# Kernel optimization log

Measured on AMD Instinct MI355X. Metric: run time of the kernel, lower is better.

Reference implementation:

```python
import jax, jax.numpy as jnp
import numpy as np

N = 1048576   # nodes (1024x1024 fluid grid)
E = 8388608   # edges (avg degree 8)
IDX_NODE_X, IDX_NODE_Y = 0, 1
IDX_EDGE_X, IDX_EDGE_Y = 0, 1


def setup_inputs() -> dict:
    key = jax.random.key(0)
    ks = jax.random.split(key, 9)
    v_x = jax.random.normal(ks[0], (N, 2), jnp.float32)
    v_prev_x = jax.random.normal(ks[1], (N, 2), jnp.float32)
    p_x = jax.random.normal(ks[2], (N, 1), jnp.float32)
    p_prev_x = jax.random.normal(ks[3], (N, 1), jnp.float32)
    rho_x = jax.random.normal(ks[4], (N, 1), jnp.float32)
    rho_prev_x = jax.random.normal(ks[5], (N, 1), jnp.float32)
    edge_attr = jax.random.normal(ks[6], (E, 2), jnp.float32)
    # mimic grid finite-difference sparsity: ~half the entries of each
    # direction column are exactly zero, exercising the != 0 edge masking
    keep = jax.random.bernoulli(ks[7], 0.5, (E, 2))
    edge_attr = jnp.where(keep, edge_attr, 0.0)
    edge_index = jax.random.randint(ks[8], (2, E), 0, N, dtype=jnp.int64)
    return dict(
        v_x=v_x, v_prev_x=v_prev_x, p_x=p_x, p_prev_x=p_prev_x,
        rho_x=rho_x, rho_prev_x=rho_prev_x,
        M=jnp.float32(1.0), eta=jnp.float32(1.0), zeta=jnp.float32(1.0),
        dt=jnp.float32(0.01), edge_attr=edge_attr, edge_index=edge_index,
    )


def _spatial_derivative(x, src, dst, edge_attr, mask, idx_node, idx_edge, n):
    """Gather-compute-scatter finite difference: scatter-mean of
    (x[dst, idx_node] - x[src, idx_node]) / edge_attr[:, idx_edge]
    over the masked edge subset, aggregated at the source node."""
    diff = x[dst, idx_node] - x[src, idx_node]                  # [E]
    denom = jnp.where(mask, edge_attr[:, idx_edge], 1.0)        # avoid /0 on masked-out edges
    contrib = jnp.where(mask, diff / denom, 0.0)                # [E]
    sums = jax.ops.segment_sum(contrib, src, num_segments=n)    # [N]
    cnt = jax.ops.segment_sum(mask.astype(x.dtype), src, num_segments=n)
    return sums / jnp.maximum(cnt, 1.0)                         # [N]


def reference(v_x, v_prev_x, p_x, p_prev_x, rho_x, rho_prev_x, M, eta, zeta, dt, edge_attr, edge_index):
    n = v_x.shape[0]
    src, dst = edge_index[0], edge_index[1]
    vp = v_x * p_x                                  # [N,2] * [N,1] -> [N,2]
    mask_x = edge_attr[:, IDX_NODE_X] != 0          # edges with x-offset
    mask_y = edge_attr[:, IDX_NODE_Y] != 0          # edges with y-offset
    d_x = _spatial_derivative(vp, src, dst, edge_attr, mask_x, IDX_NODE_X, IDX_EDGE_X, n)
    d_y = _spatial_derivative(vp, src, dst, edge_attr, mask_y, IDX_NODE_Y, IDX_EDGE_Y, n)
    loss_continuity = (d_x + d_y)[:, None] + (p_x - p_prev_x) / dt   # [N,1]
    return loss_continuity
```

## Files before the change

### kernel.cpp

```cpp
#include <hip/hip_runtime.h>
#include <hip/hip_fp16.h>


#define NPB      2048
#define NPB_LOG  11
#define NBUCK_MAX 512
#define CE       4096
#define CB       1024
#define EPT      4
#define CCAP     4608
#define MAXCHUNK 2048
#define NHINT    4096
#define SPILLCAP (1 << 20)
#define K_OFF    1073741824.0

typedef unsigned long long ull;
typedef float vfloat2 __attribute__((ext_vector_type(2)));


__global__ void node_pre_fast(const float2* __restrict__ v,
                              const float* __restrict__ p,
                              __half2* __restrict__ vph,
                              int* __restrict__ spill_cnt, int N) {
    int i = blockIdx.x * blockDim.x + threadIdx.x;
    int stride = gridDim.x * blockDim.x;
    for (; i < N; i += stride) {
        float2 vi = v[i];
        float pi = p[i];
        vph[i] = __float22half2_rn(make_float2(vi.x * pi, vi.y * pi));
    }
    if (blockIdx.x == 0 && threadIdx.x == 0) *spill_cnt = 0;
}

__device__ __forceinline__ void route_rec(uint2 r, int k, size_t rb, int slot,
                                          uint2* __restrict__ recs,
                                          uint4* __restrict__ spill,
                                          int* __restrict__ spill_cnt) {
    if (slot < CCAP) { recs[rb + slot] = r; return; }
    int sp = atomicAdd(spill_cnt, 1);
    if (sp < SPILLCAP) spill[sp] = make_uint4(r.x, r.y, (unsigned)k, 0u);
}

__global__ __launch_bounds__(CB) void chunk_sort(
        const float2* __restrict__ ea,
        const int* __restrict__ src_idx,
        const int* __restrict__ dst_idx,
        uint2* __restrict__ recs,
        unsigned short* __restrict__ off_mat,
        unsigned short* __restrict__ cnt_mat,
        uint4* __restrict__ spill,
        int* __restrict__ spill_cnt,
        int nbuck, int E) {
    __shared__ uint2 stage[CCAP];
    __shared__ int hist[NBUCK_MAX];
    __shared__ int tl[NBUCK_MAX];
    __shared__ int cur[NBUCK_MAX];
    int c = blockIdx.x, t = threadIdx.x;
    int e0 = c * CE;

    uint2 R0[EPT], R1[EPT];
    int K[EPT], NR[EPT];
#pragma unroll
    for (int i = 0; i < EPT; ++i) {
        int e = e0 + i * CB + t;
        NR[i] = 0; K[i] = 0;
        if (e < E) {
            float2 a = ea[e];
            bool mx = (a.x != 0.f);
            bool my = (a.y != 0.f);
            if (mx || my) {
                int s = src_idx[e];
                int d = dst_idx[e];
                K[i] = s >> NPB_LOG;
                unsigned sl = (unsigned)(s & (NPB - 1));
                unsigned dm = (unsigned)d << 12;
                NR[i] = (int)mx + (int)my;
                uint2 rx = make_uint2(sl | dm, __float_as_uint(a.x));
                uint2 ry = make_uint2(sl | 0x800u | dm, __float_as_uint(a.y));
                R0[i] = mx ? rx : ry;
                R1[i] = ry;
            }
        }
    }
    if (t < nbuck) hist[t] = 0;
    __syncthreads();
#pragma unroll
    for (int i = 0; i < EPT; ++i)
        if (NR[i]) atomicAdd(&hist[K[i]], NR[i]);
    __syncthreads();
    if (t < nbuck) tl[t] = hist[t];
    __syncthreads();
    for (int off = 1; off < NBUCK_MAX; off <<= 1) {
        int x = 0;
        if (t < nbuck && t >= off) x = tl[t - off];
        __syncthreads();
        if (t < nbuck) tl[t] += x;
        __syncthreads();
    }
    int total = tl[nbuck - 1];
    if (t < nbuck) {
        int excl = tl[t] - hist[t];
        cur[t] = excl;
        off_mat[(size_t)c * nbuck + t] = (unsigned short)excl;
        cnt_mat[(size_t)c * nbuck + t] = (unsigned short)hist[t];
    }
    __syncthreads();
    size_t rb = (size_t)c * CCAP;
    if (total <= CCAP) {
#pragma unroll
        for (int i = 0; i < EPT; ++i)
            if (NR[i]) {
                int slot = atomicAdd(&cur[K[i]], NR[i]);
                stage[slot] = R0[i];
                if (NR[i] == 2) stage[slot + 1] = R1[i];
            }
        __syncthreads();
        for (int j = t; j < total; j += CB) recs[rb + j] = stage[j];
    } else {
#pragma unroll
        for (int i = 0; i < EPT; ++i)
            if (NR[i]) {
                int slot = atomicAdd(&cur[K[i]], NR[i]);
                route_rec(R0[i], K[i], rb, slot, recs, spill, spill_cnt);
                if (NR[i] == 2) route_rec(R1[i], K[i], rb, slot + 1, recs, spill, spill_cnt);
            }
    }
}

__global__ __launch_bounds__(1024) void bucket_reduce(
        const uint2* __restrict__ recs,
        const unsigned short* __restrict__ off_mat,
        const unsigned short* __restrict__ cnt_mat,
        const float2* __restrict__ v,
        const float* __restrict__ p,
        const __half2* __restrict__ vph,
        const uint4* __restrict__ spill,
        const int* __restrict__ spill_cnt,
        const float* __restrict__ p_prev,
        const float* __restrict__ dt_ptr,
        float* __restrict__ out,
        int nchunk, int nbuck, int N) {
    __shared__ float2 vps[NPB];
    __shared__ double2 acc[NPB];
    __shared__ int glen[MAXCHUNK];
    __shared__ int goff[MAXCHUNK];
    __shared__ unsigned short hint[NHINT];
    __shared__ int s_sp;
    int k = blockIdx.x, t = threadIdx.x;
    int g0 = k * NPB;
    const vfloat2* vv = (const vfloat2*)v;
    for (int i = t; i < NPB; i += 1024) {
        int g = g0 + i;
        vfloat2 vi = (g < N) ? __builtin_nontemporal_load(&vv[g]) : (vfloat2)(0.f);
        float pi = (g < N) ? __builtin_nontemporal_load(&p[g]) : 0.f;
        vps[i] = make_float2(vi.x * pi, vi.y * pi);
        acc[i] = make_double2(0.0, 0.0);
    }
    if (t == 0) s_sp = *spill_cnt;
    for (int c = t; c < MAXCHUNK; c += 1024) {
        int len = 0, off = 0;
        if (c < nchunk) {
            off = __builtin_nontemporal_load(&off_mat[(size_t)c * nbuck + k]);
            int cnt = __builtin_nontemporal_load(&cnt_mat[(size_t)c * nbuck + k]);
            len = min(cnt, max(0, CCAP - off));
        }
        goff[c] = off;
        glen[c] = len;
    }
    __syncthreads();
    for (int off = 1; off < MAXCHUNK; off <<= 1) {
        int i0 = t, i1 = t + 1024;
        int x0 = (i0 >= off) ? glen[i0 - off] : 0;
        int x1 = glen[i1 - off];
        __syncthreads();
        glen[i0] += x0;
        glen[i1] += x1;
        __syncthreads();
    }
    int total = glen[MAXCHUNK - 1];
    int nh = min((total + 7) >> 3, NHINT);
    for (int j = t; j < nh; j += 1024) {
        int target = j << 3;
        int lo = 0, hi = nchunk - 1;
        while (lo < hi) {
            int mid = (lo + hi) >> 1;
            if (glen[mid] > target) hi = mid; else lo = mid + 1;
        }
        hint[j] = (unsigned short)lo;
    }
    __syncthreads();
    const ull* recs64 = (const ull*)recs;
    for (int idx = t; idx < total; idx += 1024) {
        int cur = hint[idx >> 3];
        while (glen[cur] <= idx) ++cur;
        int pre = cur ? glen[cur - 1] : 0;
        ull rv = __builtin_nontemporal_load(
            &recs64[(size_t)cur * CCAP + goff[cur] + (idx - pre)]);
        unsigned m = (unsigned)rv;
        float a = __uint_as_float((unsigned)(rv >> 32));
        int sl = (int)(m & (NPB - 1u));
        bool diry = (m >> 11) & 1u;
        int d = (int)(m >> 12);
        float2 vpd = __half22float2(vph[d]);
        float2 vs = vps[sl];
        float c = (diry ? vpd.y - vs.y : vpd.x - vs.x) / a;
        unsafeAtomicAdd(diry ? &acc[sl].y : &acc[sl].x, (double)c + K_OFF);
    }
    __syncthreads();
    int nsp = min(s_sp, SPILLCAP);
    for (int i = t; i < nsp; i += 1024) {
        uint4 r = spill[i];
        if ((int)r.z != k) continue;
        unsigned m = r.x;
        float a = __uint_as_float(r.y);
        int sl = (int)(m & (NPB - 1u));
        bool diry = (m >> 11) & 1u;
        int d = (int)(m >> 12);
        float2 vpd = __half22float2(vph[d]);
        float2 vs = vps[sl];
        float c = (diry ? vpd.y - vs.y : vpd.x - vs.x) / a;
        unsafeAtomicAdd(diry ? &acc[sl].y : &acc[sl].x, (double)c + K_OFF);
    }
    if (nsp) __syncthreads();
    float inv_dt = 1.0f / dt_ptr[0];
    for (int i = t; i < NPB; i += 1024) {
        int g = g0 + i;
        if (g < N) {
            double2 A = acc[i];
            double cx = rint(A.x * (1.0 / K_OFF));
            double sx = A.x - cx * K_OFF;
            double cy = rint(A.y * (1.0 / K_OFF));
            double sy = A.y - cy * K_OFF;
            float pd = __builtin_nontemporal_load(&p[g]);
            float pp = __builtin_nontemporal_load(&p_prev[g]);
            out[g] = (float)(sx / fmax(cx, 1.0)) + (float)(sy / fmax(cy, 1.0))
                   + (pd - pp) * inv_dt;
        }
    }
}


__global__ void fb_node_pre(const float2* __restrict__ v,
                            const float* __restrict__ p,
                            float2* __restrict__ vp,
                            double2* __restrict__ acc, int N) {
    int i = blockIdx.x * blockDim.x + threadIdx.x;
    int stride = gridDim.x * blockDim.x;
    for (; i < N; i += stride) {
        float2 vi = v[i];
        float pi = p[i];
        vp[i] = make_float2(vi.x * pi, vi.y * pi);
        acc[i] = make_double2(0.0, 0.0);
    }
}

__global__ void fb_edge_scatter(const float2* __restrict__ vp,
                                const float2* __restrict__ ea,
                                const int* __restrict__ src_idx,
                                const int* __restrict__ dst_idx,
                                double2* __restrict__ acc, int E) {
    int e = blockIdx.x * blockDim.x + threadIdx.x;
    if (e >= E) return;
    float2 a = ea[e];
    bool mx = (a.x != 0.f);
    bool my = (a.y != 0.f);
    if (!mx && !my) return;
    int s = src_idx[e];
    int d = dst_idx[e];
    float2 vs = vp[s];
    float2 vd = vp[d];
    double* basep = (double*)&acc[s];
    if (mx) unsafeAtomicAdd(basep + 0, (double)((vd.x - vs.x) / a.x) + K_OFF);
    if (my) unsafeAtomicAdd(basep + 1, (double)((vd.y - vs.y) / a.y) + K_OFF);
}

__global__ void fb_node_final(const double2* __restrict__ acc,
                              const float* __restrict__ p,
                              const float* __restrict__ p_prev,
                              const float* __restrict__ dt_ptr,
                              float* __restrict__ out, int N) {
    int i = blockIdx.x * blockDim.x + threadIdx.x;
    int stride = gridDim.x * blockDim.x;
    float inv_dt = 1.0f / dt_ptr[0];
    for (; i < N; i += stride) {
        double2 A = acc[i];
        double cx = rint(A.x * (1.0 / K_OFF));
        double sx = A.x - cx * K_OFF;
        double cy = rint(A.y * (1.0 / K_OFF));
        double sy = A.y - cy * K_OFF;
        out[i] = (float)(sx / fmax(cx, 1.0)) + (float)(sy / fmax(cy, 1.0))
               + (p[i] - p_prev[i]) * inv_dt;
    }
}


extern "C" void kernel_launch(void* const* d_in, const int* in_sizes, int n_in,
                              void* d_out, int out_size, void* d_ws, size_t ws_size,
                              hipStream_t stream) {
    const float2* v_x    = (const float2*)d_in[0];
    const float*  p_x    = (const float*)d_in[2];
    const float*  p_prev = (const float*)d_in[3];
    const float*  dt     = (const float*)d_in[9];
    const float2* ea     = (const float2*)d_in[10];
    const int*    eidx   = (const int*)d_in[11];

    const int N = in_sizes[2];
    const int E = in_sizes[10] / 2;
    const int* src_idx = eidx;
    const int* dst_idx = eidx + E;

    const int nbuck  = (N + NPB - 1) >> NPB_LOG;
    const int nchunk = (E + CE - 1) / CE;

    char* w = (char*)d_ws;
    __half2* vph      = (__half2*)w;  w += (size_t)N * sizeof(__half2);
    int*     spill_cnt= (int*)w;      w += 16;
    unsigned short* off_mat = (unsigned short*)w;  w += (size_t)nchunk * nbuck * sizeof(unsigned short);
    unsigned short* cnt_mat = (unsigned short*)w;  w += (size_t)nchunk * nbuck * sizeof(unsigned short);
    w = (char*)(((uintptr_t)w + 15) & ~(uintptr_t)15);
    uint4*   spill    = (uint4*)w;    w += (size_t)SPILLCAP * sizeof(uint4);
    uint2*   recs     = (uint2*)w;    w += (size_t)nchunk * CCAP * sizeof(uint2);
    size_t need_fast = (size_t)(w - (char*)d_ws);

    if (nbuck <= NBUCK_MAX && nchunk <= MAXCHUNK && N <= (1 << 20)
        && ws_size >= need_fast) {
        node_pre_fast<<<2048, 256, 0, stream>>>(v_x, p_x, vph, spill_cnt, N);
        chunk_sort<<<nchunk, CB, 0, stream>>>(ea, src_idx, dst_idx,
                                              recs, off_mat, cnt_mat,
                                              spill, spill_cnt, nbuck, E);
        bucket_reduce<<<nbuck, 1024, 0, stream>>>(recs, off_mat, cnt_mat,
                                                  v_x, p_x, vph,
                                                  spill, spill_cnt,
                                                  p_prev, dt,
                                                  (float*)d_out, nchunk, nbuck, N);
    } else {
        float2*  fvp  = (float2*)d_ws;
        double2* facc = (double2*)((char*)d_ws + (size_t)N * sizeof(float2));
        fb_node_pre<<<2048, 256, 0, stream>>>(v_x, p_x, fvp, facc, N);
        fb_edge_scatter<<<(E + 255) / 256, 256, 0, stream>>>(
            fvp, ea, src_idx, dst_idx, facc, E);
        fb_node_final<<<2048, 256, 0, stream>>>(
            facc, p_x, p_prev, dt, (float*)d_out, N);
    }
}
```

Before: 157.2 us.

## Pack both edge directions into one 12-byte record per edge

```diff
diff --git a/kernel.cpp b/kernel.cpp
--- a/kernel.cpp
+++ b/kernel.cpp
@@ -8,14 +8,15 @@
 #define CE       4096
 #define CB       1024
 #define EPT      4
-#define CCAP     4608
+#define CCAP     3456
 #define MAXCHUNK 2048
 #define NHINT    4096
-#define SPILLCAP (1 << 20)
+#define SPILLCAP (1 << 18)
 #define K_OFF    1073741824.0
 
 typedef unsigned long long ull;
-typedef float vfloat2 __attribute__((ext_vector_type(2)));
+
+struct __align__(4) Rec12 { unsigned m; float ax, ay; };
 
 
 __global__ void node_pre_fast(const float2* __restrict__ v,
@@ -32,33 +33,25 @@
     if (blockIdx.x == 0 && threadIdx.x == 0) *spill_cnt = 0;
 }
 
-__device__ __forceinline__ void route_rec(uint2 r, int k, size_t rb, int slot,
-                                          uint2* __restrict__ recs,
-                                          uint4* __restrict__ spill,
-                                          int* __restrict__ spill_cnt) {
-    if (slot < CCAP) { recs[rb + slot] = r; return; }
-    int sp = atomicAdd(spill_cnt, 1);
-    if (sp < SPILLCAP) spill[sp] = make_uint4(r.x, r.y, (unsigned)k, 0u);
-}
-
 __global__ __launch_bounds__(CB) void chunk_sort(
         const float2* __restrict__ ea,
         const int* __restrict__ src_idx,
         const int* __restrict__ dst_idx,
-        uint2* __restrict__ recs,
+        Rec12* __restrict__ recs,
         unsigned short* __restrict__ off_mat,
         unsigned short* __restrict__ cnt_mat,
         uint4* __restrict__ spill,
         int* __restrict__ spill_cnt,
         int nbuck, int E) {
-    __shared__ uint2 stage[CCAP];
+    __shared__ Rec12 stage[CCAP];
     __shared__ int hist[NBUCK_MAX];
     __shared__ int tl[NBUCK_MAX];
     __shared__ int cur[NBUCK_MAX];
     int c = blockIdx.x, t = threadIdx.x;
     int e0 = c * CE;
 
-    uint2 R0[EPT], R1[EPT];
+    unsigned M[EPT];
+    float AX[EPT], AY[EPT];
     int K[EPT], NR[EPT];
 #pragma unroll
     for (int i = 0; i < EPT; ++i) {
@@ -66,19 +59,14 @@
         NR[i] = 0; K[i] = 0;
         if (e < E) {
             float2 a = ea[e];
-            bool mx = (a.x != 0.f);
-            bool my = (a.y != 0.f);
-            if (mx || my) {
+            if (a.x != 0.f || a.y != 0.f) {
                 int s = src_idx[e];
                 int d = dst_idx[e];
                 K[i] = s >> NPB_LOG;
-                unsigned sl = (unsigned)(s & (NPB - 1));
-                unsigned dm = (unsigned)d << 12;
-                NR[i] = (int)mx + (int)my;
-                uint2 rx = make_uint2(sl | dm, __float_as_uint(a.x));
-                uint2 ry = make_uint2(sl | 0x800u | dm, __float_as_uint(a.y));
-                R0[i] = mx ? rx : ry;
-                R1[i] = ry;
+                M[i] = (unsigned)(s & (NPB - 1)) | ((unsigned)d << NPB_LOG);
+                AX[i] = a.x;
+                AY[i] = a.y;
+                NR[i] = 1;
             }
         }
     }
@@ -86,7 +74,7 @@
     __syncthreads();
 #pragma unroll
     for (int i = 0; i < EPT; ++i)
-        if (NR[i]) atomicAdd(&hist[K[i]], NR[i]);
+        if (NR[i]) atomicAdd(&hist[K[i]], 1);
     __syncthreads();
     if (t < nbuck) tl[t] = hist[t];
     __syncthreads();
@@ -110,9 +98,10 @@
 #pragma unroll
         for (int i = 0; i < EPT; ++i)
             if (NR[i]) {
-                int slot = atomicAdd(&cur[K[i]], NR[i]);
-                stage[slot] = R0[i];
-                if (NR[i] == 2) stage[slot + 1] = R1[i];
+                int slot = atomicAdd(&cur[K[i]], 1);
+                stage[slot].m = M[i];
+                stage[slot].ax = AX[i];
+                stage[slot].ay = AY[i];
             }
         __syncthreads();
         for (int j = t; j < total; j += CB) recs[rb + j] = stage[j];
@@ -120,15 +109,23 @@
 #pragma unroll
         for (int i = 0; i < EPT; ++i)
             if (NR[i]) {
-                int slot = atomicAdd(&cur[K[i]], NR[i]);
-                route_rec(R0[i], K[i], rb, slot, recs, spill, spill_cnt);
-                if (NR[i] == 2) route_rec(R1[i], K[i], rb, slot + 1, recs, spill, spill_cnt);
+                int slot = atomicAdd(&cur[K[i]], 1);
+                if (slot < CCAP) {
+                    recs[rb + slot].m = M[i];
+                    recs[rb + slot].ax = AX[i];
+                    recs[rb + slot].ay = AY[i];
+                } else {
+                    int sp = atomicAdd(spill_cnt, 1);
+                    if (sp < SPILLCAP)
+                        spill[sp] = make_uint4(M[i], __float_as_uint(AX[i]),
+                                               __float_as_uint(AY[i]), (unsigned)K[i]);
+                }
             }
     }
 }
 
 __global__ __launch_bounds__(1024) void bucket_reduce(
-        const uint2* __restrict__ recs,
+        const Rec12* __restrict__ recs,
         const unsigned short* __restrict__ off_mat,
         const unsigned short* __restrict__ cnt_mat,
         const float2* __restrict__ v,
@@ -148,11 +145,10 @@
     __shared__ int s_sp;
     int k = blockIdx.x, t = threadIdx.x;
     int g0 = k * NPB;
-    const vfloat2* vv = (const vfloat2*)v;
     for (int i = t; i < NPB; i += 1024) {
         int g = g0 + i;
-        vfloat2 vi = (g < N) ? __builtin_nontemporal_load(&vv[g]) : (vfloat2)(0.f);
-        float pi = (g < N) ? __builtin_nontemporal_load(&p[g]) : 0.f;
+        float2 vi = (g < N) ? v[g] : make_float2(0.f, 0.f);
+        float pi = (g < N) ? p[g] : 0.f;
         vps[i] = make_float2(vi.x * pi, vi.y * pi);
         acc[i] = make_double2(0.0, 0.0);
     }
@@ -160,8 +156,8 @@
     for (int c = t; c < MAXCHUNK; c += 1024) {
         int len = 0, off = 0;
         if (c < nchunk) {
-            off = __builtin_nontemporal_load(&off_mat[(size_t)c * nbuck + k]);
-            int cnt = __builtin_nontemporal_load(&cnt_mat[(size_t)c * nbuck + k]);
+            off = off_mat[(size_t)c * nbuck + k];
+            int cnt = cnt_mat[(size_t)c * nbuck + k];
             len = min(cnt, max(0, CCAP - off));
         }
         goff[c] = off;
@@ -189,37 +185,35 @@
         hint[j] = (unsigned short)lo;
     }
     __syncthreads();
-    const ull* recs64 = (const ull*)recs;
     for (int idx = t; idx < total; idx += 1024) {
         int cur = hint[idx >> 3];
         while (glen[cur] <= idx) ++cur;
         int pre = cur ? glen[cur - 1] : 0;
-        ull rv = __builtin_nontemporal_load(
-            &recs64[(size_t)cur * CCAP + goff[cur] + (idx - pre)]);
-        unsigned m = (unsigned)rv;
-        float a = __uint_as_float((unsigned)(rv >> 32));
-        int sl = (int)(m & (NPB - 1u));
-        bool diry = (m >> 11) & 1u;
-        int d = (int)(m >> 12);
+        Rec12 r = recs[(size_t)cur * CCAP + goff[cur] + (idx - pre)];
+        int sl = (int)(r.m & (NPB - 1u));
+        int d = (int)(r.m >> NPB_LOG);
         float2 vpd = __half22float2(vph[d]);
         float2 vs = vps[sl];
-        float c = (diry ? vpd.y - vs.y : vpd.x - vs.x) / a;
-        unsafeAtomicAdd(diry ? &acc[sl].y : &acc[sl].x, (double)c + K_OFF);
+        if (r.ax != 0.f)
+            unsafeAtomicAdd(&acc[sl].x, (double)((vpd.x - vs.x) / r.ax) + K_OFF);
+        if (r.ay != 0.f)
+            unsafeAtomicAdd(&acc[sl].y, (double)((vpd.y - vs.y) / r.ay) + K_OFF);
     }
     __syncthreads();
     int nsp = min(s_sp, SPILLCAP);
     for (int i = t; i < nsp; i += 1024) {
         uint4 r = spill[i];
-        if ((int)r.z != k) continue;
-        unsigned m = r.x;
-        float a = __uint_as_float(r.y);
-        int sl = (int)(m & (NPB - 1u));
-        bool diry = (m >> 11) & 1u;
-        int d = (int)(m >> 12);
+        if ((int)r.w != k) continue;
+        int sl = (int)(r.x & (NPB - 1u));
+        int d = (int)(r.x >> NPB_LOG);
+        float ax = __uint_as_float(r.y);
+        float ay = __uint_as_float(r.z);
         float2 vpd = __half22float2(vph[d]);
         float2 vs = vps[sl];
-        float c = (diry ? vpd.y - vs.y : vpd.x - vs.x) / a;
-        unsafeAtomicAdd(diry ? &acc[sl].y : &acc[sl].x, (double)c + K_OFF);
+        if (ax != 0.f)
+            unsafeAtomicAdd(&acc[sl].x, (double)((vpd.x - vs.x) / ax) + K_OFF);
+        if (ay != 0.f)
+            unsafeAtomicAdd(&acc[sl].y, (double)((vpd.y - vs.y) / ay) + K_OFF);
     }
     if (nsp) __syncthreads();
     float inv_dt = 1.0f / dt_ptr[0];
@@ -231,10 +225,8 @@
             double sx = A.x - cx * K_OFF;
             double cy = rint(A.y * (1.0 / K_OFF));
             double sy = A.y - cy * K_OFF;
-            float pd = __builtin_nontemporal_load(&p[g]);
-            float pp = __builtin_nontemporal_load(&p_prev[g]);
             out[g] = (float)(sx / fmax(cx, 1.0)) + (float)(sy / fmax(cy, 1.0))
-                   + (pd - pp) * inv_dt;
+                   + (p[g] - p_prev[g]) * inv_dt;
         }
     }
 }
@@ -319,7 +311,7 @@
     unsigned short* cnt_mat = (unsigned short*)w;  w += (size_t)nchunk * nbuck * sizeof(unsigned short);
     w = (char*)(((uintptr_t)w + 15) & ~(uintptr_t)15);
     uint4*   spill    = (uint4*)w;    w += (size_t)SPILLCAP * sizeof(uint4);
-    uint2*   recs     = (uint2*)w;    w += (size_t)nchunk * CCAP * sizeof(uint2);
+    Rec12*   recs     = (Rec12*)w;    w += (size_t)nchunk * CCAP * sizeof(Rec12);
     size_t need_fast = (size_t)(w - (char*)d_ws);
 
     if (nbuck <= NBUCK_MAX && nchunk <= MAXCHUNK && N <= (1 << 20)
```

Result: faster. 131.1 us (median of 2 runs) (-16.6%).
